# Performance work log

Measured on AMD Instinct MI355X. Metric: run time of the kernel, lower is better.

Reference implementation:

```python
import jax, jax.numpy as jnp
import numpy as np

B, S, D = 4, 8192, 1024


def setup_inputs() -> dict:
    key = jax.random.key(0)
    kx, kb = jax.random.split(key)
    x = jax.random.normal(kx, (B, S, D), dtype=jnp.float32)
    boundaries = jax.random.bernoulli(kb, 0.25, (B, S))  # bool mask
    return {"x": x, "boundaries": boundaries}


def reference(x, boundaries):
    # x: [B, S, D], boundaries: [B, S] bool
    batch, seq_len, dim = x.shape
    num_tokens = boundaries.sum(axis=-1)                      # [B] int
    # max_chunks is data-dependent; evaluated eagerly (as in the torch module's int())
    max_chunks = int(jnp.max(num_tokens))
    # boundary tokens keep their index; non-boundary tokens get +seq_len so a
    # stable argsort compacts boundary tokens to the front, preserving order.
    token_idx = jnp.arange(seq_len)[None, :] + (~boundaries).astype(jnp.int32) * seq_len
    seq_sorted_indices = jnp.argsort(token_idx, axis=1, stable=True)  # [B, S]
    sel = seq_sorted_indices[:, :max_chunks]                  # [B, max_chunks]
    next_hidden_states = jnp.take_along_axis(x, sel[:, :, None], axis=1)  # [B, max_chunks, D]
    return next_hidden_states, num_tokens
```

## Files before the change

### kernel.cpp

```cpp
#include <hip/hip_runtime.h>

#define BB 4
#define SS 8192
#define DD 1024
#define TPB 1024
#define GROUP 64

typedef float vf4 __attribute__((ext_vector_type(4)));

__global__ __launch_bounds__(TPB) void chunk_block(const void* __restrict__ bptr,
                                                   const float* __restrict__ x,
                                                   float* __restrict__ out,
                                                   float* __restrict__ ntok,
                                                   int max_chunks, int ngroups) {
    const int b = blockIdx.x / ngroups;
    const int g = blockIdx.x % ngroups;
    const int row0 = g * GROUP;
    const int t = threadIdx.x;
    const int lane = t & 63;
    const int wave = t >> 6;

    int f;
    {
        const uint4* __restrict__ wp = (const uint4*)bptr;
        uint4 w = wp[lane];
        unsigned int o = w.x | w.y | w.z | w.w;
        const bool non = __any((o & 0xFEFEFEFEu) != 0u);
        const bool mis = __any((o & 0xFFFFFF00u) != 0u);
        f = non ? 2 : (mis ? 1 : 0);
    }

    unsigned int mask = 0;
    if (f == 0) {
        const int4* __restrict__ p = (const int4*)((const int*)bptr + b * SS);
        int4 w0 = p[t * 2], w1 = p[t * 2 + 1];
        int vi[8] = {w0.x, w0.y, w0.z, w0.w, w1.x, w1.y, w1.z, w1.w};
        #pragma unroll
        for (int k = 0; k < 8; ++k) mask |= (unsigned int)(vi[k] != 0) << k;
    } else if (f == 1) {
        const uint2* __restrict__ p = (const uint2*)((const unsigned char*)bptr + b * SS);
        uint2 w = p[t];
        unsigned int ws[2] = {w.x, w.y};
        #pragma unroll
        for (int k = 0; k < 8; ++k)
            mask |= (unsigned int)(((ws[k >> 2] >> ((k & 3) * 8)) & 0xFFu) != 0u) << k;
    } else {
        const float4* __restrict__ p = (const float4*)((const float*)bptr + b * SS);
        float4 w0 = p[t * 2], w1 = p[t * 2 + 1];
        float vf[8] = {w0.x, w0.y, w0.z, w0.w, w1.x, w1.y, w1.z, w1.w};
        #pragma unroll
        for (int k = 0; k < 8; ++k) mask |= (unsigned int)(vf[k] != 0.0f) << k;
    }
    const int cnt = __popc(mask);

    int scan = cnt;
    #pragma unroll
    for (int o = 1; o < 64; o <<= 1) {
        int n = __shfl_up(scan, o, 64);
        if (lane >= o) scan += n;
    }

    __shared__ int waveTot[16];
    __shared__ int s_rowj[GROUP];
    if (lane == 63) waveTot[wave] = scan;
    __syncthreads();
    int waveOff = 0, T = 0;
    #pragma unroll
    for (int w = 0; w < 16; ++w) {
        const int wt = waveTot[w];
        waveOff += (w < wave) ? wt : 0;
        T += wt;
    }

    int tr = waveOff + (scan - cnt);
    #pragma unroll
    for (int k = 0; k < 8; ++k) {
        const int j = t * 8 + k;
        int dest;
        if ((mask >> k) & 1u) { dest = tr; tr++; }
        else                  { dest = T + (j - tr); }
        const int rel = dest - row0;
        if ((unsigned)rel < (unsigned)GROUP) s_rowj[rel] = j;
    }
    if (g == 0 && t == 0) ntok[b] = (float)T;
    __syncthreads();

    const int rbase = wave * 4;
    const vf4* src[4];
    vf4* dst[4];
    bool valid[4];
    #pragma unroll
    for (int r = 0; r < 4; ++r) {
        const int c = row0 + rbase + r;
        valid[r] = c < max_chunks;
        const int cc = valid[r] ? c : 0;
        const int j = s_rowj[valid[r] ? (rbase + r) : 0];
        src[r] = (const vf4*)(x + ((long long)b * SS + j) * DD);
        dst[r] = (vf4*)(out + ((long long)b * max_chunks + cc) * (long long)DD);
    }
    vf4 v[4][4];
    #pragma unroll
    for (int r = 0; r < 4; ++r)
        #pragma unroll
        for (int q = 0; q < 4; ++q)
            v[r][q] = src[r][lane + 64 * q];
    #pragma unroll
    for (int r = 0; r < 4; ++r)
        if (valid[r])
            #pragma unroll
            for (int q = 0; q < 4; ++q)
                dst[r][lane + 64 * q] = v[r][q];
}

extern "C" void kernel_launch(void* const* d_in, const int* in_sizes, int n_in,
                              void* d_out, int out_size, void* d_ws, size_t ws_size,
                              hipStream_t stream) {
    const float* x = (const float*)d_in[0];
    const void* bptr = d_in[1];
    float* out = (float*)d_out;

    const int max_chunks = (out_size - BB) / (BB * DD);
    const int ngroups = (max_chunks + GROUP - 1) / GROUP;
    float* ntok = out + (long long)BB * max_chunks * DD;

    chunk_block<<<BB * ngroups, TPB, 0, stream>>>(bptr, x, out, ntok, max_chunks, ngroups);
}
```

Baseline: 18.12 us.

## Compute per-wave compaction indices with wave-local scan and rank selection

Each wave now scans the whole boundary row on its own (64 lanes × 128 elements) and finds the source row for each output by ballot plus a binary search for the nth set bit. This removes both block-wide __syncthreads, the shared-memory wave totals and the scatter into shared memory, so waves can start their gather independently. In exchange every wave reads the full mask row, with up to 32 vector loads per lane, and does extra ALU work for the rank lookup.

```diff
diff --git a/kernel.cpp b/kernel.cpp
--- a/kernel.cpp
+++ b/kernel.cpp
@@ -5,8 +5,30 @@
 #define DD 1024
 #define TPB 1024
 #define GROUP 64
+#define LPL 128
 
 typedef float vf4 __attribute__((ext_vector_type(4)));
+
+__device__ __forceinline__ int nth_set_u32(unsigned int w, int r) {
+    int p = 0;
+    #pragma unroll
+    for (int step = 16; step >= 1; step >>= 1) {
+        const unsigned int lm = (p + step >= 32) ? 0xFFFFFFFFu : ((1u << (p + step)) - 1u);
+        if (__popc(w & lm) <= r) p += step;
+    }
+    return p;
+}
+
+__device__ __forceinline__ int nth_set_128(unsigned int m0, unsigned int m1,
+                                           unsigned int m2, unsigned int m3, int r) {
+    const int c0 = __popc(m0), c1 = __popc(m1), c2 = __popc(m2);
+    unsigned int w; int base;
+    if (r < c0)                { w = m0; base = 0; }
+    else if (r < c0 + c1)      { w = m1; base = 32; r -= c0; }
+    else if (r < c0 + c1 + c2) { w = m2; base = 64; r -= c0 + c1; }
+    else                       { w = m3; base = 96; r -= c0 + c1 + c2; }
+    return base + nth_set_u32(w, r);
+}
 
 __global__ __launch_bounds__(TPB) void chunk_block(const void* __restrict__ bptr,
                                                    const float* __restrict__ x,
@@ -30,74 +52,92 @@
         f = non ? 2 : (mis ? 1 : 0);
     }
 
-    unsigned int mask = 0;
-    if (f == 0) {
-        const int4* __restrict__ p = (const int4*)((const int*)bptr + b * SS);
-        int4 w0 = p[t * 2], w1 = p[t * 2 + 1];
-        int vi[8] = {w0.x, w0.y, w0.z, w0.w, w1.x, w1.y, w1.z, w1.w};
+    unsigned int m0 = 0, m1 = 0, m2 = 0, m3 = 0;
+    if (f == 1) {
+        const uint4* __restrict__ p =
+            (const uint4*)((const unsigned char*)bptr + b * SS + lane * LPL);
+        unsigned int mm[4] = {0, 0, 0, 0};
         #pragma unroll
-        for (int k = 0; k < 8; ++k) mask |= (unsigned int)(vi[k] != 0) << k;
-    } else if (f == 1) {
-        const uint2* __restrict__ p = (const uint2*)((const unsigned char*)bptr + b * SS);
-        uint2 w = p[t];
-        unsigned int ws[2] = {w.x, w.y};
+        for (int r8 = 0; r8 < 8; ++r8) {
+            uint4 w = p[r8];
+            unsigned int ws[4] = {w.x, w.y, w.z, w.w};
+            unsigned int bits16 = 0;
+            #pragma unroll
+            for (int q = 0; q < 4; ++q) {
+                unsigned int v = ws[q];
+                unsigned int tt = v | (v >> 4); tt |= tt >> 2; tt |= tt >> 1;
+                const unsigned int nib = (((tt & 0x01010101u) * 0x01020408u) >> 24) & 0xFu;
+                bits16 |= nib << (q * 4);
+            }
+            mm[r8 >> 1] |= bits16 << ((r8 & 1) * 16);
+        }
+        m0 = mm[0]; m1 = mm[1]; m2 = mm[2]; m3 = mm[3];
+    } else if (f == 0) {
+        const uint4* __restrict__ p = (const uint4*)((const int*)bptr + b * SS + lane * LPL);
+        unsigned int mm[4] = {0, 0, 0, 0};
         #pragma unroll
-        for (int k = 0; k < 8; ++k)
-            mask |= (unsigned int)(((ws[k >> 2] >> ((k & 3) * 8)) & 0xFFu) != 0u) << k;
+        for (int r4 = 0; r4 < 32; ++r4) {
+            uint4 w = p[r4];
+            const unsigned int nib = (unsigned int)((w.x != 0) | ((w.y != 0) << 1) |
+                                                    ((w.z != 0) << 2) | ((w.w != 0) << 3));
+            mm[r4 >> 3] |= nib << ((r4 & 7) * 4);
+        }
+        m0 = mm[0]; m1 = mm[1]; m2 = mm[2]; m3 = mm[3];
     } else {
-        const float4* __restrict__ p = (const float4*)((const float*)bptr + b * SS);
-        float4 w0 = p[t * 2], w1 = p[t * 2 + 1];
-        float vf[8] = {w0.x, w0.y, w0.z, w0.w, w1.x, w1.y, w1.z, w1.w};
+        const float4* __restrict__ p =
+            (const float4*)((const float*)bptr + b * SS + lane * LPL);
+        unsigned int mm[4] = {0, 0, 0, 0};
         #pragma unroll
-        for (int k = 0; k < 8; ++k) mask |= (unsigned int)(vf[k] != 0.0f) << k;
+        for (int r4 = 0; r4 < 32; ++r4) {
+            float4 w = p[r4];
+            const unsigned int nib = (unsigned int)((w.x != 0.0f) | ((w.y != 0.0f) << 1) |
+                                                    ((w.z != 0.0f) << 2) | ((w.w != 0.0f) << 3));
+            mm[r4 >> 3] |= nib << ((r4 & 7) * 4);
+        }
+        m0 = mm[0]; m1 = mm[1]; m2 = mm[2]; m3 = mm[3];
     }
-    const int cnt = __popc(mask);
 
+    const int cnt = __popc(m0) + __popc(m1) + __popc(m2) + __popc(m3);
     int scan = cnt;
     #pragma unroll
     for (int o = 1; o < 64; o <<= 1) {
         int n = __shfl_up(scan, o, 64);
         if (lane >= o) scan += n;
     }
+    const int tb = scan - cnt;
+    const int T = __shfl(scan, 63);
+    const int fb = lane * LPL - tb;
 
-    __shared__ int waveTot[16];
-    __shared__ int s_rowj[GROUP];
-    if (lane == 63) waveTot[wave] = scan;
-    __syncthreads();
-    int waveOff = 0, T = 0;
-    #pragma unroll
-    for (int w = 0; w < 16; ++w) {
-        const int wt = waveTot[w];
-        waveOff += (w < wave) ? wt : 0;
-        T += wt;
-    }
+    if (g == 0 && t == 0) ntok[b] = (float)T;
 
-    int tr = waveOff + (scan - cnt);
-    #pragma unroll
-    for (int k = 0; k < 8; ++k) {
-        const int j = t * 8 + k;
-        int dest;
-        if ((mask >> k) & 1u) { dest = tr; tr++; }
-        else                  { dest = T + (j - tr); }
-        const int rel = dest - row0;
-        if ((unsigned)rel < (unsigned)GROUP) s_rowj[rel] = j;
-    }
-    if (g == 0 && t == 0) ntok[b] = (float)T;
-    __syncthreads();
-
-    const int rbase = wave * 4;
     const vf4* src[4];
     vf4* dst[4];
     bool valid[4];
     #pragma unroll
     for (int r = 0; r < 4; ++r) {
-        const int c = row0 + rbase + r;
+        const int c = row0 + wave * 4 + r;
         valid[r] = c < max_chunks;
         const int cc = valid[r] ? c : 0;
-        const int j = s_rowj[valid[r] ? (rbase + r) : 0];
+        int j;
+        if (cc < T) {
+            const int rk = cc;
+            const bool own = (tb <= rk) && (rk < tb + cnt);
+            const unsigned long long bal = __ballot(own);
+            const int owner = __ffsll((unsigned long long)bal) - 1;
+            const int jl = lane * LPL + nth_set_128(m0, m1, m2, m3, rk - tb);
+            j = __shfl(jl, owner);
+        } else {
+            const int rk = cc - T;
+            const bool own = (fb <= rk) && (rk < fb + (LPL - cnt));
+            const unsigned long long bal = __ballot(own);
+            const int owner = __ffsll((unsigned long long)bal) - 1;
+            const int jl = lane * LPL + nth_set_128(~m0, ~m1, ~m2, ~m3, rk - fb);
+            j = __shfl(jl, owner);
+        }
         src[r] = (const vf4*)(x + ((long long)b * SS + j) * DD);
         dst[r] = (vf4*)(out + ((long long)b * max_chunks + cc) * (long long)DD);
     }
+
     vf4 v[4][4];
     #pragma unroll
     for (int r = 0; r < 4; ++r)
```

Result: slower. 29.02 us (+60.1%).
